# Kernel tuning notes

Hardware: AMD Instinct MI355X
Metric: run time of the kernel (lower is better)

The kernel has to match this reference:

```python
import jax, jax.numpy as jnp
import numpy as np

DIM = 384
FRACTION = 16   # quant_bits=16 -> fixed-point fraction bits
INTEGER = 16
WEIGHT_BITS = 5
SHIFT_MIN = -(2 ** (WEIGHT_BITS - 1) - 2)  # -14 (DeepShift shift_range for 5-bit)


def _ste(x, qx):
    # straight-through estimator: forward qx, backward identity
    return x + jax.lax.stop_gradient(qx - x)


def _clampabs(w, mn, mx):
    # clamp |w| into [mn, mx], preserving sign (zeros stay zero)
    return jnp.sign(w) * jnp.clip(jnp.abs(w), mn, mx)


def _round_power_of_2(w):
    # w -> sign(w) * 2^round(log2(|w|))
    shift = jnp.round(jnp.log2(jnp.maximum(jnp.abs(w), 1e-30)))
    return jnp.sign(w) * jnp.exp2(shift)


def _round_to_fixed(x, fraction=FRACTION, integer=INTEGER):
    delta = 2.0 ** (-fraction)
    bound = 2.0 ** (integer - 1)
    return jnp.clip(jnp.floor(x / delta) * delta, -bound, bound - 1)


def setup_inputs() -> dict:
    key = jax.random.key(0)
    k1, k2, k3 = jax.random.split(key, 3)
    x = jax.random.normal(k1, (32, DIM, 56, 56), dtype=jnp.float32)
    weight = jax.random.normal(k2, (DIM, 1, 3, 3), dtype=jnp.float32) * 0.1
    bias = jax.random.normal(k3, (DIM,), dtype=jnp.float32) * 0.01
    return {"x": x, "weight": weight, "bias": bias}


def reference(x, weight, bias):
    # weight: clamp magnitude to [2^-14, 2^0], then round to signed power of two (5-bit shift)
    w = _ste(weight, _clampabs(weight, 2.0 ** SHIFT_MIN, 1.0))
    w = _ste(w, _round_power_of_2(w))
    # activations / bias: 16-bit fixed-point rounding
    xq = _ste(x, _round_to_fixed(x))
    bq = _ste(bias, _round_to_fixed(bias))
    # depthwise 3x3 conv, stride 1, padding 1, groups = DIM
    out = jax.lax.conv_general_dilated(
        xq, w,
        window_strides=(1, 1),
        padding=((1, 1), (1, 1)),
        feature_group_count=DIM,
        dimension_numbers=("NCHW", "OIHW", "NCHW"),
    )
    return out + bq[None, :, None, None]
```

## Files before the change

### kernel.cpp

```cpp
#include <hip/hip_runtime.h>


#define DW_C   384
#define DW_H   56
#define DW_W   56
#define DW_HW  (DW_H * DW_W)
#define DW_HW4 (DW_HW / 4)
#define DW_W4  (DW_W / 4)

__device__ __forceinline__ float qfix(float v) {
    v = floorf(v * 65536.0f) * (1.0f / 65536.0f);
    return fminf(fmaxf(v, -32768.0f), 32767.0f);
}

__global__ __launch_bounds__(256) void peg_shift_dwconv(
    const float* __restrict__ x, const float* __restrict__ wgt,
    const float* __restrict__ bias, float* __restrict__ out)
{
    __shared__ float s[DW_HW];

    const int plane = blockIdx.x;
    const int c = plane % DW_C;
    const float* xp = x + (size_t)plane * DW_HW;
    float* op = out + (size_t)plane * DW_HW;

    const float4* xp4 = (const float4*)xp;
    float4* s4 = (float4*)s;
    for (int i = threadIdx.x; i < DW_HW4; i += 256) {
        float4 v = xp4[i];
        v.x = qfix(v.x); v.y = qfix(v.y); v.z = qfix(v.z); v.w = qfix(v.w);
        s4[i] = v;
    }

    float wq[9];
#pragma unroll
    for (int k = 0; k < 9; ++k) {
        float wv = wgt[c * 9 + k];
        float aw = fabsf(wv);
        float cw = fminf(fmaxf(aw, 6.103515625e-05f ), 1.0f);
        float q  = exp2f(rintf(log2f(cw)));
        wq[k] = (wv > 0.0f) ? q : ((wv < 0.0f) ? -q : 0.0f);
    }
    float bq = qfix(bias[c]);

    __syncthreads();

    for (int iv = threadIdx.x; iv < DW_HW4; iv += 256) {
        int h  = iv / DW_W4;
        int w0 = (iv - h * DW_W4) * 4;
        float a0 = bq, a1 = bq, a2 = bq, a3 = bq;
#pragma unroll
        for (int dh = 0; dh < 3; ++dh) {
            int hh = h + dh - 1;
            if (hh < 0 || hh >= DW_H) continue;
            const float* row = s + hh * DW_W;
            float4 m = *(const float4*)(row + w0);
            float left  = (w0 > 0)        ? row[w0 - 1] : 0.0f;
            float right = (w0 < DW_W - 4) ? row[w0 + 4] : 0.0f;
            float wl = wq[dh * 3 + 0], wm = wq[dh * 3 + 1], wr = wq[dh * 3 + 2];
            a0 += left * wl + m.x * wm + m.y * wr;
            a1 += m.x  * wl + m.y * wm + m.z * wr;
            a2 += m.y  * wl + m.z * wm + m.w * wr;
            a3 += m.z  * wl + m.w * wm + right * wr;
        }
        float4 o; o.x = a0; o.y = a1; o.z = a2; o.w = a3;
        ((float4*)op)[iv] = o;
    }
}

extern "C" void kernel_launch(void* const* d_in, const int* in_sizes, int n_in,
                              void* d_out, int out_size, void* d_ws, size_t ws_size,
                              hipStream_t stream) {
    const float* x = (const float*)d_in[0];
    const float* w = (const float*)d_in[1];
    const float* b = (const float*)d_in[2];
    float* out = (float*)d_out;

    int planes = in_sizes[0] / DW_HW;
    peg_shift_dwconv<<<planes, 256, 0, stream>>>(x, w, b, out);
}
```

Measured before the change: 270.3 us.

## Process eight planes per block with double-buffered LDS prefetch and padded rows

Each block now handles eight consecutive planes instead of one. The next plane's global loads are issued into registers before the current plane is computed, then written to a second LDS buffer, so load latency overlaps with compute. LDS rows are padded with zero halo columns, which removes the border branches, and the accumulation uses explicit fmaf. The trade-offs are fewer blocks (1536), higher register pressure from holding the prefetch, and a launch that assumes the plane count is divisible by eight.

```diff
diff --git a/kernel.cpp b/kernel.cpp
--- a/kernel.cpp
+++ b/kernel.cpp
@@ -4,67 +4,124 @@
 #define DW_C   384
 #define DW_H   56
 #define DW_W   56
-#define DW_HW  (DW_H * DW_W)
-#define DW_HW4 (DW_HW / 4)
-#define DW_W4  (DW_W / 4)
+#define DW_HW  3136
+#define DW_HW4 784
+#define DW_W4  14
+#define LDS_STRIDE 60
+#define LDS_SIZE (DW_H * LDS_STRIDE + 4)
+#define PPB 8
 
 __device__ __forceinline__ float qfix(float v) {
     v = floorf(v * 65536.0f) * (1.0f / 65536.0f);
     return fminf(fmaxf(v, -32768.0f), 32767.0f);
 }
 
-__global__ __launch_bounds__(256) void peg_shift_dwconv(
+__device__ __forceinline__ float4 qfix4(float4 v) {
+    v.x = qfix(v.x); v.y = qfix(v.y); v.z = qfix(v.z); v.w = qfix(v.w);
+    return v;
+}
+
+__global__ __launch_bounds__(256, 6) void peg_shift_dwconv(
     const float* __restrict__ x, const float* __restrict__ wgt,
     const float* __restrict__ bias, float* __restrict__ out)
 {
-    __shared__ float s[DW_HW];
+    __shared__ float s[2][LDS_SIZE];
 
-    const int plane = blockIdx.x;
-    const int c = plane % DW_C;
-    const float* xp = x + (size_t)plane * DW_HW;
-    float* op = out + (size_t)plane * DW_HW;
+    const int tid = threadIdx.x;
+    const int p0  = blockIdx.x * PPB;
 
-    const float4* xp4 = (const float4*)xp;
-    float4* s4 = (float4*)s;
-    for (int i = threadIdx.x; i < DW_HW4; i += 256) {
-        float4 v = xp4[i];
-        v.x = qfix(v.x); v.y = qfix(v.y); v.z = qfix(v.z); v.w = qfix(v.w);
-        s4[i] = v;
+    int h[4], o[4];
+#pragma unroll
+    for (int j = 0; j < 4; ++j) {
+        int iv = tid + j * 256;
+        if (iv > DW_HW4 - 1) iv = DW_HW4 - 1;
+        int hh = iv / DW_W4;
+        int w4 = iv - hh * DW_W4;
+        h[j] = hh;
+        o[j] = hh * LDS_STRIDE + 4 + w4 * 4;
     }
 
-    float wq[9];
-#pragma unroll
-    for (int k = 0; k < 9; ++k) {
-        float wv = wgt[c * 9 + k];
-        float aw = fabsf(wv);
-        float cw = fminf(fmaxf(aw, 6.103515625e-05f ), 1.0f);
-        float q  = exp2f(rintf(log2f(cw)));
-        wq[k] = (wv > 0.0f) ? q : ((wv < 0.0f) ? -q : 0.0f);
+    if (tid < DW_H) {
+        s[0][tid * LDS_STRIDE + 3]  = 0.0f;
+        s[0][tid * LDS_STRIDE + 60] = 0.0f;
+        s[1][tid * LDS_STRIDE + 3]  = 0.0f;
+        s[1][tid * LDS_STRIDE + 60] = 0.0f;
     }
-    float bq = qfix(bias[c]);
 
+    {
+        const float4* xp4 = (const float4*)(x + (size_t)p0 * DW_HW);
+        float4 r0 = xp4[tid], r1 = xp4[tid + 256], r2 = xp4[tid + 512], r3;
+        if (tid < 16) r3 = xp4[tid + 768];
+        *(float4*)(&s[0][o[0]]) = qfix4(r0);
+        *(float4*)(&s[0][o[1]]) = qfix4(r1);
+        *(float4*)(&s[0][o[2]]) = qfix4(r2);
+        if (tid < 16) *(float4*)(&s[0][o[3]]) = qfix4(r3);
+    }
     __syncthreads();
 
-    for (int iv = threadIdx.x; iv < DW_HW4; iv += 256) {
-        int h  = iv / DW_W4;
-        int w0 = (iv - h * DW_W4) * 4;
-        float a0 = bq, a1 = bq, a2 = bq, a3 = bq;
+    float* cur = s[0];
+    float* nxt = s[1];
+
 #pragma unroll
-        for (int dh = 0; dh < 3; ++dh) {
-            int hh = h + dh - 1;
-            if (hh < 0 || hh >= DW_H) continue;
-            const float* row = s + hh * DW_W;
-            float4 m = *(const float4*)(row + w0);
-            float left  = (w0 > 0)        ? row[w0 - 1] : 0.0f;
-            float right = (w0 < DW_W - 4) ? row[w0 + 4] : 0.0f;
-            float wl = wq[dh * 3 + 0], wm = wq[dh * 3 + 1], wr = wq[dh * 3 + 2];
-            a0 += left * wl + m.x * wm + m.y * wr;
-            a1 += m.x  * wl + m.y * wm + m.z * wr;
-            a2 += m.y  * wl + m.z * wm + m.w * wr;
-            a3 += m.z  * wl + m.w * wm + right * wr;
+    for (int k = 0; k < PPB; ++k) {
+        const bool more = (k + 1 < PPB);
+
+        float4 r0, r1, r2, r3;
+        if (more) {
+            const float4* np4 = (const float4*)(x + (size_t)(p0 + k + 1) * DW_HW);
+            r0 = np4[tid]; r1 = np4[tid + 256]; r2 = np4[tid + 512];
+            if (tid < 16) r3 = np4[tid + 768];
         }
-        float4 o; o.x = a0; o.y = a1; o.z = a2; o.w = a3;
-        ((float4*)op)[iv] = o;
+
+        const int c = (p0 + k) % DW_C;
+        const float* wp = wgt + c * 9;
+        float wq[9];
+#pragma unroll
+        for (int t = 0; t < 9; ++t) {
+            float wv = wp[t];
+            float aw = fabsf(wv);
+            float cw = fminf(fmaxf(aw, 6.103515625e-05f ), 1.0f);
+            float q  = exp2f(rintf(log2f(cw)));
+            wq[t] = (wv > 0.0f) ? q : ((wv < 0.0f) ? -q : 0.0f);
+        }
+        const float bq = qfix(bias[c]);
+
+        float4* op4 = (float4*)(out + (size_t)(p0 + k) * DW_HW);
+
+#define ROWFMA(RP, W0, W1, W2) {                                      \
+            const float* rp_ = (RP);                                  \
+            float4 m_ = *(const float4*)rp_;                          \
+            float L_ = rp_[-1], R_ = rp_[4];                          \
+            a0 = fmaf(L_,   W0, fmaf(m_.x, W1, fmaf(m_.y, W2, a0))); \
+            a1 = fmaf(m_.x, W0, fmaf(m_.y, W1, fmaf(m_.z, W2, a1))); \
+            a2 = fmaf(m_.y, W0, fmaf(m_.z, W1, fmaf(m_.w, W2, a2))); \
+            a3 = fmaf(m_.z, W0, fmaf(m_.w, W1, fmaf(R_,   W2, a3))); }
+
+#define COMPUTE(J) {                                                  \
+            float a0 = bq, a1 = bq, a2 = bq, a3 = bq;                 \
+            const float* base = cur + o[J];                           \
+            if (h[J] > 0)        ROWFMA(base - LDS_STRIDE, wq[0], wq[1], wq[2]); \
+            ROWFMA(base, wq[3], wq[4], wq[5]);                        \
+            if (h[J] < DW_H - 1) ROWFMA(base + LDS_STRIDE, wq[6], wq[7], wq[8]); \
+            float4 ov_; ov_.x = a0; ov_.y = a1; ov_.z = a2; ov_.w = a3; \
+            op4[tid + (J) * 256] = ov_; }
+
+        COMPUTE(0)
+        COMPUTE(1)
+        COMPUTE(2)
+        if (tid < 16) COMPUTE(3)
+
+#undef COMPUTE
+#undef ROWFMA
+
+        if (more) {
+            *(float4*)(&nxt[o[0]]) = qfix4(r0);
+            *(float4*)(&nxt[o[1]]) = qfix4(r1);
+            *(float4*)(&nxt[o[2]]) = qfix4(r2);
+            if (tid < 16) *(float4*)(&nxt[o[3]]) = qfix4(r3);
+        }
+        __syncthreads();
+        float* t_ = cur; cur = nxt; nxt = t_;
     }
 }
 
@@ -77,5 +134,6 @@
     float* out = (float*)d_out;
 
     int planes = in_sizes[0] / DW_HW;
-    peg_shift_dwconv<<<planes, 256, 0, stream>>>(x, w, b, out);
+    int nblocks = planes / PPB;
+    peg_shift_dwconv<<<nblocks, 256, 0, stream>>>(x, w, b, out);
 }
```

Result: slower. 285.1 us (+5.5%).

## Replace LDS tiling with per-thread column streaming and precomputed quantized weights

Applied to the files above, without the earlier changes.

Drops the shared-memory plane tile. Each thread now owns a 4-wide column strip over 28 rows and slides a register window of three rows down it, loading one new row per output row straight from global memory. Weight and bias quantization moves into a small separate kernel that writes to workspace, so the main kernel only loads the ready values. This removes the LDS staging and the block barrier and lets many more waves run at once. In exchange, adjacent threads issue uncoalesced halo loads, and there is an extra kernel launch.

```diff
diff --git a/kernel.cpp b/kernel.cpp
--- a/kernel.cpp
+++ b/kernel.cpp
@@ -1,70 +1,128 @@
 #include <hip/hip_runtime.h>
 
 
-#define DW_C   384
-#define DW_H   56
-#define DW_W   56
-#define DW_HW  (DW_H * DW_W)
-#define DW_HW4 (DW_HW / 4)
-#define DW_W4  (DW_W / 4)
+#define DW_C     384
+#define DW_H     56
+#define DW_W     56
+#define DW_HW    3136
+#define SEG_ROWS 28
+#define NW4      14
 
 __device__ __forceinline__ float qfix(float v) {
     v = floorf(v * 65536.0f) * (1.0f / 65536.0f);
     return fminf(fmaxf(v, -32768.0f), 32767.0f);
 }
 
-__global__ __launch_bounds__(256) void peg_shift_dwconv(
-    const float* __restrict__ x, const float* __restrict__ wgt,
-    const float* __restrict__ bias, float* __restrict__ out)
+struct Row { float l, a, b, c, d, r; };
+
+__global__ __launch_bounds__(256) void quant_wb(
+    const float* __restrict__ wgt, const float* __restrict__ bias,
+    float* __restrict__ wq, float* __restrict__ bq)
 {
-    __shared__ float s[DW_HW];
-
-    const int plane = blockIdx.x;
-    const int c = plane % DW_C;
-    const float* xp = x + (size_t)plane * DW_HW;
-    float* op = out + (size_t)plane * DW_HW;
-
-    const float4* xp4 = (const float4*)xp;
-    float4* s4 = (float4*)s;
-    for (int i = threadIdx.x; i < DW_HW4; i += 256) {
-        float4 v = xp4[i];
-        v.x = qfix(v.x); v.y = qfix(v.y); v.z = qfix(v.z); v.w = qfix(v.w);
-        s4[i] = v;
-    }
-
-    float wq[9];
-#pragma unroll
-    for (int k = 0; k < 9; ++k) {
-        float wv = wgt[c * 9 + k];
+    int i = blockIdx.x * 256 + threadIdx.x;
+    if (i < DW_C * 9) {
+        float wv = wgt[i];
         float aw = fabsf(wv);
         float cw = fminf(fmaxf(aw, 6.103515625e-05f ), 1.0f);
         float q  = exp2f(rintf(log2f(cw)));
-        wq[k] = (wv > 0.0f) ? q : ((wv < 0.0f) ? -q : 0.0f);
+        wq[i] = (wv > 0.0f) ? q : ((wv < 0.0f) ? -q : 0.0f);
     }
-    float bq = qfix(bias[c]);
+    if (i < DW_C) bq[i] = qfix(bias[i]);
+}
 
-    __syncthreads();
+template<bool PRE>
+__global__ __launch_bounds__(256, 6) void peg_shift_stream(
+    const float* __restrict__ x, const float* __restrict__ wgt,
+    const float* __restrict__ bias, float* __restrict__ out,
+    const float* __restrict__ wsq, const float* __restrict__ wsb)
+{
+    const int task = blockIdx.x * 256 + threadIdx.x;
+    const int plane = task / 28;
+    const int t28   = task - plane * 28;
+    const int seg   = t28 / NW4;
+    const int w4    = t28 - seg * NW4;
+    const int c     = plane % DW_C;
+    const int r0    = seg * SEG_ROWS;
 
-    for (int iv = threadIdx.x; iv < DW_HW4; iv += 256) {
-        int h  = iv / DW_W4;
-        int w0 = (iv - h * DW_W4) * 4;
-        float a0 = bq, a1 = bq, a2 = bq, a3 = bq;
+    const bool hl = (w4 > 0);
+    const bool hr = (w4 < NW4 - 1);
+
+    float ww[9];
+    float bqv;
+    if (PRE) {
+        const float* wp = wsq + c * 9;
 #pragma unroll
-        for (int dh = 0; dh < 3; ++dh) {
-            int hh = h + dh - 1;
-            if (hh < 0 || hh >= DW_H) continue;
-            const float* row = s + hh * DW_W;
-            float4 m = *(const float4*)(row + w0);
-            float left  = (w0 > 0)        ? row[w0 - 1] : 0.0f;
-            float right = (w0 < DW_W - 4) ? row[w0 + 4] : 0.0f;
-            float wl = wq[dh * 3 + 0], wm = wq[dh * 3 + 1], wr = wq[dh * 3 + 2];
-            a0 += left * wl + m.x * wm + m.y * wr;
-            a1 += m.x  * wl + m.y * wm + m.z * wr;
-            a2 += m.y  * wl + m.z * wm + m.w * wr;
-            a3 += m.z  * wl + m.w * wm + right * wr;
+        for (int t = 0; t < 9; ++t) ww[t] = wp[t];
+        bqv = wsb[c];
+    } else {
+        const float* wp = wgt + c * 9;
+#pragma unroll
+        for (int t = 0; t < 9; ++t) {
+            float wv = wp[t];
+            float aw = fabsf(wv);
+            float cw = fminf(fmaxf(aw, 6.103515625e-05f), 1.0f);
+            float q  = exp2f(rintf(log2f(cw)));
+            ww[t] = (wv > 0.0f) ? q : ((wv < 0.0f) ? -q : 0.0f);
         }
-        float4 o; o.x = a0; o.y = a1; o.z = a2; o.w = a3;
-        ((float4*)op)[iv] = o;
+        bqv = qfix(bias[c]);
+    }
+
+    const float* xb = x + (size_t)plane * DW_HW + w4 * 4;
+
+    auto loadq = [&](int rr) -> Row {
+        Row q;
+        if (rr >= 0 && rr < DW_H) {
+            const float* p = xb + rr * DW_W;
+            float4 m = *(const float4*)p;
+            float lv = hl ? p[-1] : 0.0f;
+            float rv = hr ? p[4]  : 0.0f;
+            q.l = qfix(lv); q.a = qfix(m.x); q.b = qfix(m.y);
+            q.c = qfix(m.z); q.d = qfix(m.w); q.r = qfix(rv);
+        } else {
+            q.l = q.a = q.b = q.c = q.d = q.r = 0.0f;
+        }
+        return q;
+    };
+
+    Row A = loadq(r0 - 1);
+    Row B = loadq(r0);
+    Row C = loadq(r0 + 1);
+
+    float* ob = out + (size_t)plane * DW_HW + r0 * DW_W + w4 * 4;
+
+#pragma unroll 4
+    for (int i = 0; i < SEG_ROWS; ++i) {
+        const int rr = r0 + i + 2;
+        float4 pm; pm.x = pm.y = pm.z = pm.w = 0.0f;
+        float pl = 0.0f, pr = 0.0f;
+        if (rr < DW_H) {
+            const float* p = xb + rr * DW_W;
+            pm = *(const float4*)p;
+            if (hl) pl = p[-1];
+            if (hr) pr = p[4];
+        }
+
+        float o0 = bqv, o1 = bqv, o2 = bqv, o3 = bqv;
+        o0 = fmaf(A.l, ww[0], fmaf(A.a, ww[1], fmaf(A.b, ww[2], o0)));
+        o1 = fmaf(A.a, ww[0], fmaf(A.b, ww[1], fmaf(A.c, ww[2], o1)));
+        o2 = fmaf(A.b, ww[0], fmaf(A.c, ww[1], fmaf(A.d, ww[2], o2)));
+        o3 = fmaf(A.c, ww[0], fmaf(A.d, ww[1], fmaf(A.r, ww[2], o3)));
+        o0 = fmaf(B.l, ww[3], fmaf(B.a, ww[4], fmaf(B.b, ww[5], o0)));
+        o1 = fmaf(B.a, ww[3], fmaf(B.b, ww[4], fmaf(B.c, ww[5], o1)));
+        o2 = fmaf(B.b, ww[3], fmaf(B.c, ww[4], fmaf(B.d, ww[5], o2)));
+        o3 = fmaf(B.c, ww[3], fmaf(B.d, ww[4], fmaf(B.r, ww[5], o3)));
+        o0 = fmaf(C.l, ww[6], fmaf(C.a, ww[7], fmaf(C.b, ww[8], o0)));
+        o1 = fmaf(C.a, ww[6], fmaf(C.b, ww[7], fmaf(C.c, ww[8], o1)));
+        o2 = fmaf(C.b, ww[6], fmaf(C.c, ww[7], fmaf(C.d, ww[8], o2)));
+        o3 = fmaf(C.c, ww[6], fmaf(C.d, ww[7], fmaf(C.r, ww[8], o3)));
+
+        float4 ov; ov.x = o0; ov.y = o1; ov.z = o2; ov.w = o3;
+        *(float4*)ob = ov;
+        ob += DW_W;
+
+        A = B; B = C;
+        C.l = qfix(pl);   C.a = qfix(pm.x); C.b = qfix(pm.y);
+        C.c = qfix(pm.z); C.d = qfix(pm.w); C.r = qfix(pr);
     }
 }
 
@@ -76,6 +134,17 @@
     const float* b = (const float*)d_in[2];
     float* out = (float*)d_out;
 
-    int planes = in_sizes[0] / DW_HW;
-    peg_shift_dwconv<<<planes, 256, 0, stream>>>(x, w, b, out);
+    int planes  = in_sizes[0] / DW_HW;
+    int tasks   = planes * 28;
+    int nblocks = (tasks + 255) / 256;
+
+    size_t need = (size_t)(DW_C * 9 + DW_C) * sizeof(float);
+    if (d_ws && ws_size >= need) {
+        float* wq = (float*)d_ws;
+        float* bq = wq + DW_C * 9;
+        quant_wb<<<(DW_C * 9 + 255) / 256, 256, 0, stream>>>(w, b, wq, bq);
+        peg_shift_stream<true><<<nblocks, 256, 0, stream>>>(x, w, b, out, wq, bq);
+    } else {
+        peg_shift_stream<false><<<nblocks, 256, 0, stream>>>(x, w, b, out, nullptr, nullptr);
+    }
 }
```

Result: slower. 307.6 us (+13.8%).
